# Optimization experiments

Measured on AMD Instinct MI355X. Metric: run time of the kernel, lower is better.

## Reference

```python
import jax, jax.numpy as jnp
import numpy as np

BN_EPS = 1e-5
DIST_EPS = 1e-8


def setup_inputs() -> dict:
    key = jax.random.key(0)
    ks = jax.random.split(key, 8)
    B, N, S = 8, 8192, 2048
    D_unk, D_kn = 128, 256
    inp = {
        "unknown_xyz": jax.random.uniform(ks[0], (B, N, 3), dtype=jnp.float32),
        "known_xyz": jax.random.uniform(ks[1], (B, S, 3), dtype=jnp.float32),
        "unknown_points": jax.random.normal(ks[2], (B, N, D_unk), dtype=jnp.float32),
        "known_points": jax.random.normal(ks[3], (B, S, D_kn), dtype=jnp.float32),
        "W0": jax.random.normal(ks[4], (256, 384), dtype=jnp.float32) * (1.0 / np.sqrt(384)),
        "b0": jnp.zeros((256,), jnp.float32),
        "g0": jnp.ones((256,), jnp.float32),
        "beta0": jnp.zeros((256,), jnp.float32),
        "W1": jax.random.normal(ks[5], (128, 256), dtype=jnp.float32) * (1.0 / np.sqrt(256)),
        "b1": jnp.zeros((128,), jnp.float32),
        "g1": jnp.ones((128,), jnp.float32),
        "beta1": jnp.zeros((128,), jnp.float32),
    }
    return inp


def _three_nn(unknown_xyz, known_xyz):
    # squared pairwise distances [B, N, S]
    d = jnp.sum((unknown_xyz[:, :, None, :] - known_xyz[:, None, :, :]) ** 2, axis=-1)
    neg_top, idx = jax.lax.top_k(-d, 3)  # 3 smallest distances
    return -neg_top, idx  # dists [B,N,3], idx [B,N,3]


def _conv_bn_relu(x, W, b, g, beta):
    # x: [B, N, Cin]; 1x1 Conv1d == per-point linear
    y = jnp.einsum("bnc,oc->bno", x, W) + b
    mean = jnp.mean(y, axis=(0, 1))
    var = jnp.var(y, axis=(0, 1))  # biased, as BatchNorm training forward
    y = g * (y - mean) * jax.lax.rsqrt(var + BN_EPS) + beta
    return jax.nn.relu(y)


def reference(unknown_xyz, known_xyz, unknown_points, known_points,
              W0, b0, g0, beta0, W1, b1, g1, beta1):
    dists, idx = _three_nn(unknown_xyz, known_xyz)
    dist_recip = 1.0 / (dists + DIST_EPS)
    weight = dist_recip / jnp.sum(dist_recip, axis=2, keepdims=True)  # [B,N,3]
    # gather 3 neighbor features: [B,N,3,D_kn]
    gathered = jax.vmap(lambda f, i: f[i])(known_points, idx)
    interpolated = jnp.sum(weight[..., None] * gathered, axis=2)  # [B,N,D_kn]
    x = jnp.concatenate([unknown_points, interpolated], axis=-1)  # [B,N,384]
    x = _conv_bn_relu(x, W0, b0, g0, beta0)
    x = _conv_bn_relu(x, W1, b1, g1, beta1)
    return x  # [B, N, 128]
```

## Files before the change

kernel.cpp:

```cpp
#include <hip/hip_runtime.h>
#include <hip/hip_bf16.h>


typedef __attribute__((ext_vector_type(8))) short short8;
typedef __attribute__((ext_vector_type(4))) float f32x4;

#define BB 8
#define NN 8192
#define SS 2048
#define M_TOT (BB * NN)
#define N1DIM 256
#define K2DIM 256
#define N2DIM 128
#define BK 64

#define GDIM 5
#define NCELL (GDIM * GDIM * GDIM)
#define SLOTS 32
#define CELLW 0.2f

#define KEY_MASK 0xFFFFF800u
#define IDX_MASK 0x7FFu

__device__ __forceinline__ unsigned short f2bf(float f) {
    unsigned int x = __float_as_uint(f);
    unsigned int r = x + 0x7fffu + ((x >> 16) & 1u);
    return (unsigned short)(r >> 16);
}
__device__ __forceinline__ float bf2f(unsigned short u) {
    return __uint_as_float(((unsigned int)u) << 16);
}
__device__ __forceinline__ unsigned int med3_u32(unsigned int a, unsigned int b,
                                                 unsigned int c) {
    unsigned int r;
    asm("v_med3_u32 %0, %1, %2, %3" : "=v"(r) : "v"(a), "v"(b), "v"(c));
    return r;
}

__device__ __forceinline__ void ins5(unsigned int k[5], unsigned int key) {
    unsigned int n1 = med3_u32(k[0], k[1], key);
    unsigned int n2 = med3_u32(k[1], k[2], key);
    unsigned int n3 = med3_u32(k[2], k[3], key);
    unsigned int n4 = med3_u32(k[3], k[4], key);
    k[0] = min(k[0], key);
    k[1] = n1; k[2] = n2; k[3] = n3; k[4] = n4;
}

__device__ __forceinline__ float rescue_write(
    const unsigned int k[5], float qx, float qy, float qz,
    const float4* __restrict__ kpB, uint4* __restrict__ widx, size_t pt)
{
    unsigned long long e[5];
#pragma unroll
    for (int i = 0; i < 5; ++i) {
        if ((k[i] & KEY_MASK) >= 0x7F800000u) {
            e[i] = 0xFFFFFFFFFFFFFFFFull;
        } else {
            unsigned int idx = k[i] & IDX_MASK;
            float4 c = kpB[idx];
            float dx = c.x - qx, dy = c.y - qy, dz = c.z - qz;
            float d = fmaf(dx, dx, fmaf(dy, dy, dz * dz));
            e[i] = ((unsigned long long)__float_as_uint(d) << 32) | idx;
        }
    }
#pragma unroll
    for (int i = 0; i < 3; ++i)
#pragma unroll
        for (int j = i + 1; j < 5; ++j)
            if (e[j] < e[i]) { unsigned long long t = e[i]; e[i] = e[j]; e[j] = t; }

    float d0 = __uint_as_float((unsigned int)(e[0] >> 32));
    float d1 = __uint_as_float((unsigned int)(e[1] >> 32));
    float d2 = __uint_as_float((unsigned int)(e[2] >> 32));
    float r0 = 1.0f / (d0 + 1e-8f);
    float r1 = 1.0f / (d1 + 1e-8f);
    float r2 = 1.0f / (d2 + 1e-8f);
    float rs = 1.0f / (r0 + r1 + r2);
    unsigned int i0 = (unsigned int)(e[0] & IDX_MASK);
    unsigned int i1 = (unsigned int)(e[1] & IDX_MASK);
    unsigned int i2 = (unsigned int)(e[2] & IDX_MASK);
    widx[pt] = make_uint4(__float_as_uint(r0 * rs), __float_as_uint(r1 * rs),
                          i0 | (i1 << 16), i2);
    return d2;
}

__device__ __forceinline__ void gload_lds16(const void* g, void* lds) {
    __builtin_amdgcn_global_load_lds(
        (const __attribute__((address_space(1))) unsigned int*)g,
        (__attribute__((address_space(3))) unsigned int*)lds, 16, 0, 0);
}

__global__ __launch_bounds__(256) void cvt_w_kernel(
    const float* __restrict__ W0, const float* __restrict__ W1,
    const float* __restrict__ kxyz,
    unsigned short* __restrict__ Wa, unsigned short* __restrict__ Wb,
    unsigned short* __restrict__ Wb1, float4* __restrict__ kpack,
    float4* __restrict__ table, int* __restrict__ cnt,
    int* __restrict__ nfail, float* __restrict__ statsF)
{
    int i = blockIdx.x * 256 + threadIdx.x;
    if (blockIdx.x == 0) {
        for (int j = threadIdx.x; j < 768; j += 256) statsF[j] = 0.0f;
        if (threadIdx.x == 0) *nfail = 0;
    }
    if (i < BB * NCELL) cnt[i] = 0;
    if (i < BB * NCELL * SLOTS)
        table[i] = make_float4(1e30f, 1e30f, 1e30f, 0.0f);
    if (i < 256 * 384) {
        int o = i / 384, c = i - o * 384;
        unsigned short v = f2bf(W0[i]);
        if (c < 128) Wa[o * 128 + c] = v;
        else         Wb[o * 256 + (c - 128)] = v;
    }
    if (i < N2DIM * K2DIM) Wb1[i] = f2bf(W1[i]);
    if (i < BB * SS) {
        const float* p = kxyz + (size_t)i * 3;
        float px = p[0], py = p[1], pz = p[2];
        kpack[i] = make_float4(px, py, pz, fmaf(px, px, fmaf(py, py, pz * pz)));
    }
}

__global__ __launch_bounds__(256) void bin_scatter_kernel(
    const float* __restrict__ kxyz, float4* __restrict__ table,
    int* __restrict__ cnt)
{
    int i = blockIdx.x * 256 + threadIdx.x;
    if (i >= BB * SS) return;
    int b = i >> 11, s = i & 2047;
    const float* p = kxyz + (size_t)i * 3;
    float x = p[0], y = p[1], z = p[2];
    int cx = min((int)(x * GDIM), GDIM - 1);
    int cy = min((int)(y * GDIM), GDIM - 1);
    int cz = min((int)(z * GDIM), GDIM - 1);
    int cell = (cz * GDIM + cy) * GDIM + cx;
    int slot = atomicAdd(&cnt[b * NCELL + cell], 1);
    if (slot < SLOTS)
        table[((size_t)(b * NCELL + cell)) * SLOTS + slot] =
            make_float4(x, y, z, __int_as_float(s));
}

__global__ __launch_bounds__(256) void nn_grid_kernel(
    const float* __restrict__ uxyz, const float4* __restrict__ table,
    const int* __restrict__ cnt, const float4* __restrict__ kpack,
    uint4* __restrict__ widx, int* __restrict__ fail_list,
    int* __restrict__ nfail)
{
    const int t  = blockIdx.x * 256 + threadIdx.x;
    const int qd = t & 3;
    const size_t pt = (size_t)(t >> 2);
    const int b = (int)(pt >> 13);

    const float* up = uxyz + pt * 3;
    const float qx = up[0], qy = up[1], qz = up[2];

    const int cx = min((int)(qx * GDIM), GDIM - 1);
    const int cy = min((int)(qy * GDIM), GDIM - 1);
    const int cz = min((int)(qz * GDIM), GDIM - 1);
    const float fx = qx * GDIM - cx, fy = qy * GDIM - cy, fz = qz * GDIM - cz;
    int ox = cx - (fx <= 0.5f ? 1 : 0); ox = max(0, min(ox, GDIM - 2));
    int oy = cy - (fy <= 0.5f ? 1 : 0); oy = max(0, min(oy, GDIM - 2));
    int oz = cz - (fz <= 0.5f ? 1 : 0); oz = max(0, min(oz, GDIM - 2));

    const float4* tb = table + (size_t)b * NCELL * SLOTS;
    const int* cb = cnt + b * NCELL;

    unsigned int k[5] = {0xFFFFFFFFu, 0xFFFFFFFFu, 0xFFFFFFFFu,
                         0xFFFFFFFFu, 0xFFFFFFFFu};
    int ovf = 0;
#pragma unroll
    for (int jj = 0; jj < 2; ++jj) {
        const int j = qd * 2 + jj;
        const int dx = j & 1, dy = (j >> 1) & 1, dz = j >> 2;
        const int cell = ((oz + dz) * GDIM + (oy + dy)) * GDIM + (ox + dx);
        ovf |= (cb[cell] > SLOTS) ? 1 : 0;
        const float4* cp = tb + (size_t)cell * SLOTS;
#pragma unroll 8
        for (int s = 0; s < SLOTS; ++s) {
            float4 c = cp[s];
            float ddx = c.x - qx, ddy = c.y - qy, ddz = c.z - qz;
            float d = fmaf(ddx, ddx, fmaf(ddy, ddy, ddz * ddz));
            unsigned int key = (__float_as_uint(d) & KEY_MASK) |
                               (unsigned int)__float_as_int(c.w);
            ins5(k, key);
        }
    }

#pragma unroll
    for (int m = 1; m <= 2; m <<= 1) {
        unsigned int f0 = (unsigned int)__shfl_xor((int)k[0], m);
        unsigned int f1 = (unsigned int)__shfl_xor((int)k[1], m);
        unsigned int f2 = (unsigned int)__shfl_xor((int)k[2], m);
        unsigned int f3 = (unsigned int)__shfl_xor((int)k[3], m);
        unsigned int f4 = (unsigned int)__shfl_xor((int)k[4], m);
        ovf |= __shfl_xor(ovf, m);
        ins5(k, f0); ins5(k, f1); ins5(k, f2); ins5(k, f3); ins5(k, f4);
    }

    if (qd != 0) return;

    float d3 = rescue_write(k, qx, qy, qz, kpack + (size_t)b * SS, widx, pt);

    float lx = ox * CELLW, rx = (ox + 2) * CELLW;
    float ly = oy * CELLW, ry = (oy + 2) * CELLW;
    float lz = oz * CELLW, rz = (oz + 2) * CELLW;
    float covx = fminf(ox == 0 ? 1e30f : qx - lx, ox == GDIM - 2 ? 1e30f : rx - qx);
    float covy = fminf(oy == 0 ? 1e30f : qy - ly, oy == GDIM - 2 ? 1e30f : ry - qy);
    float covz = fminf(oz == 0 ? 1e30f : qz - lz, oz == GDIM - 2 ? 1e30f : rz - qz);
    float g = fminf(covx, fminf(covy, covz));

    if (ovf || !(d3 <= g * g)) {
        int pos = atomicAdd(nfail, 1);
        fail_list[pos] = (int)pt;
    }
}

__global__ __launch_bounds__(256) void nn_brute_kernel(
    const float* __restrict__ uxyz, const float4* __restrict__ kpack,
    const int* __restrict__ fail_list, const int* __restrict__ nfail,
    uint4* __restrict__ widx)
{
    const int l = threadIdx.x & 63;
    const int wv = (blockIdx.x * 256 + threadIdx.x) >> 6;
    const int nw = (gridDim.x * 256) >> 6;
    const int n = *nfail;

    for (int q = wv; q < n; q += nw) {
        const size_t pt = (size_t)fail_list[q];
        const int b = (int)(pt >> 13);
        const float* up = uxyz + pt * 3;
        const float qx = up[0], qy = up[1], qz = up[2];
        const float4* kp = kpack + (size_t)b * SS;

        unsigned int k[5] = {0xFFFFFFFFu, 0xFFFFFFFFu, 0xFFFFFFFFu,
                             0xFFFFFFFFu, 0xFFFFFFFFu};
#pragma unroll 4
        for (int s = l; s < SS; s += 64) {
            float4 c = kp[s];
            float ddx = c.x - qx, ddy = c.y - qy, ddz = c.z - qz;
            float d = fmaf(ddx, ddx, fmaf(ddy, ddy, ddz * ddz));
            unsigned int key = (__float_as_uint(d) & KEY_MASK) | (unsigned int)s;
            ins5(k, key);
        }
#pragma unroll
        for (int m = 1; m <= 32; m <<= 1) {
            unsigned int f0 = (unsigned int)__shfl_xor((int)k[0], m);
            unsigned int f1 = (unsigned int)__shfl_xor((int)k[1], m);
            unsigned int f2 = (unsigned int)__shfl_xor((int)k[2], m);
            unsigned int f3 = (unsigned int)__shfl_xor((int)k[3], m);
            unsigned int f4 = (unsigned int)__shfl_xor((int)k[4], m);
            ins5(k, f0); ins5(k, f1); ins5(k, f2); ins5(k, f3); ins5(k, f4);
        }
        if (l == 0)
            rescue_write(k, qx, qy, qz, kp, widx, pt);
    }
}

__global__ __launch_bounds__(512, 4) void zgemm_kernel(
    const float* __restrict__ kpts,
    const unsigned short* __restrict__ Wb,
    unsigned short* __restrict__ Z)
{
    __shared__ __align__(128) unsigned char smem[2 * 32768];

    const int tid = threadIdx.x;
    const int l = tid & 63, w = tid >> 6;
    const int wm = w >> 2, wn = w & 3;
    const int mt = blockIdx.x >> 1, nh = blockIdx.x & 1;
    const int row0 = mt * 128;
    const int srow = l >> 3, sbo = (l & 7) * 16;
    const int lr = tid >> 2, lcq = tid & 3;

    f32x4 acc[4][2];
#pragma unroll
    for (int m = 0; m < 4; ++m)
#pragma unroll
        for (int n = 0; n < 2; ++n) {
            f32x4 z = {0.f, 0.f, 0.f, 0.f};
            acc[m][n] = z;
        }

    const unsigned char* Bb = (const unsigned char*)Wb + (size_t)nh * 128 * 512;
    float4 af0, af1, af2, af3;

    auto issueA = [&](int t) {
        const float* src = kpts + (size_t)(row0 + lr) * 256 + t * 64 + lcq * 16;
        af0 = ((const float4*)src)[0];
        af1 = ((const float4*)src)[1];
        af2 = ((const float4*)src)[2];
        af3 = ((const float4*)src)[3];
    };
    auto stageB = [&](int buf, int t) {
        unsigned char* Bl = smem + buf * 32768 + 16384;
#pragma unroll
        for (int i = 0; i < 2; ++i) {
            const int r = w * 16 + i * 8 + srow;
            gload_lds16(Bb + (size_t)r * 512 + t * 128 + (sbo ^ ((r & 7) << 4)),
                        Bl + r * 128 + sbo);
        }
    };
    auto xformA = [&](int buf) {
        unsigned char* Al = smem + buf * 32768;
        short8 o0, o1;
        o0[0] = (short)f2bf(af0.x); o0[1] = (short)f2bf(af0.y);
        o0[2] = (short)f2bf(af0.z); o0[3] = (short)f2bf(af0.w);
        o0[4] = (short)f2bf(af1.x); o0[5] = (short)f2bf(af1.y);
        o0[6] = (short)f2bf(af1.z); o0[7] = (short)f2bf(af1.w);
        o1[0] = (short)f2bf(af2.x); o1[1] = (short)f2bf(af2.y);
        o1[2] = (short)f2bf(af2.z); o1[3] = (short)f2bf(af2.w);
        o1[4] = (short)f2bf(af3.x); o1[5] = (short)f2bf(af3.y);
        o1[6] = (short)f2bf(af3.z); o1[7] = (short)f2bf(af3.w);
        const int bo = lcq * 32;
        *(short8*)(Al + lr * 128 + ((bo) ^ ((lr & 7) << 4))) = o0;
        *(short8*)(Al + lr * 128 + ((bo + 16) ^ ((lr & 7) << 4))) = o1;
    };
    auto compute = [&](int buf) {
        const unsigned char* Al = smem + buf * 32768;
        const unsigned char* Bl = Al + 16384;
#pragma unroll
        for (int ks = 0; ks < 2; ++ks) {
            const int bo = ks * 64 + (l >> 4) * 16;
            short8 a[4], bq[2];
#pragma unroll
            for (int m = 0; m < 4; ++m) {
                const int r = wm * 64 + m * 16 + (l & 15);
                a[m] = *(const short8*)(Al + r * 128 + (bo ^ ((r & 7) << 4)));
            }
#pragma unroll
            for (int n = 0; n < 2; ++n) {
                const int r = wn * 32 + n * 16 + (l & 15);
                bq[n] = *(const short8*)(Bl + r * 128 + (bo ^ ((r & 7) << 4)));
            }
#pragma unroll
            for (int m = 0; m < 4; ++m)
#pragma unroll
                for (int n = 0; n < 2; ++n)
                    acc[m][n] = __builtin_amdgcn_mfma_f32_16x16x32_bf16(
                        a[m], bq[n], acc[m][n], 0, 0, 0);
        }
    };

    issueA(0);
    stageB(0, 0);
    xformA(0);
    __syncthreads();
#pragma unroll
    for (int t = 0; t < 4; ++t) {
        const int cur = t & 1;
        if (t + 1 < 4) { issueA(t + 1); stageB(cur ^ 1, t + 1); }
        compute(cur);
        if (t + 1 < 4) xformA(cur ^ 1);
        __syncthreads();
    }

#pragma unroll
    for (int m = 0; m < 4; ++m) {
        const int row = row0 + wm * 64 + m * 16 + (l >> 4) * 4;
#pragma unroll
        for (int n = 0; n < 2; ++n) {
            const int col = nh * 128 + wn * 32 + n * 16 + (l & 15);
            f32x4 v = acc[m][n];
#pragma unroll
            for (int r = 0; r < 4; ++r)
                Z[(size_t)(row + r) * 256 + col] = f2bf(v[r]);
        }
    }
}

__global__ __launch_bounds__(256) void interp_z_kernel(
    const uint4* __restrict__ widx,
    const unsigned short* __restrict__ Z,
    unsigned short* __restrict__ xz)
{
    __shared__ int   sidx[64][3];
    __shared__ float sw[64][3];

    const int tid = threadIdx.x;
    const int bid = blockIdx.x;
    const int b   = bid & 7;
    const int pn  = (bid >> 3) * 64;

    if (tid < 64) {
        uint4 wv = widx[(size_t)b * NN + pn + tid];
        float w0 = __uint_as_float(wv.x);
        float w1 = __uint_as_float(wv.y);
        sidx[tid][0] = (int)(wv.z & 0xFFFFu);
        sidx[tid][1] = (int)(wv.z >> 16);
        sidx[tid][2] = (int)wv.w;
        sw[tid][0] = w0; sw[tid][1] = w1; sw[tid][2] = 1.0f - w0 - w1;
    }
    __syncthreads();

    const int wvv = tid >> 6, lane = tid & 63;
    const unsigned short* Zb = Z + (size_t)b * SS * 256;
    for (int p = wvv; p < 64; p += 4) {
        const int j0 = sidx[p][0], j1 = sidx[p][1], j2 = sidx[p][2];
        const float w0 = sw[p][0], w1 = sw[p][1], w2 = sw[p][2];

        ushort4 z0 = *(const ushort4*)(Zb + (size_t)j0 * 256 + lane * 4);
        ushort4 z1 = *(const ushort4*)(Zb + (size_t)j1 * 256 + lane * 4);
        ushort4 z2 = *(const ushort4*)(Zb + (size_t)j2 * 256 + lane * 4);
        ushort4 o;
        o.x = f2bf(fmaf(w2, bf2f(z2.x), fmaf(w1, bf2f(z1.x), w0 * bf2f(z0.x))));
        o.y = f2bf(fmaf(w2, bf2f(z2.y), fmaf(w1, bf2f(z1.y), w0 * bf2f(z0.y))));
        o.z = f2bf(fmaf(w2, bf2f(z2.z), fmaf(w1, bf2f(z1.z), w0 * bf2f(z0.z))));
        o.w = f2bf(fmaf(w2, bf2f(z2.w), fmaf(w1, bf2f(z1.w), w0 * bf2f(z0.w))));
        *(ushort4*)(xz + ((size_t)b * NN + pn + p) * 256 + lane * 4) = o;
    }
}

__global__ __launch_bounds__(512, 4) void gemm1z_kernel(
    const float* __restrict__ upts,
    const unsigned short* __restrict__ Wa,
    const unsigned short* __restrict__ xz,
    unsigned short* __restrict__ Y0,
    float* __restrict__ stats)
{
    __shared__ __align__(128) unsigned char smem[65536];

    const int tid = threadIdx.x;
    const int l = tid & 63, w = tid >> 6;
    const int wm = w >> 2, wn = w & 3;
    const int mt = blockIdx.x >> 1, nh = blockIdx.x & 1;
    const int row0 = mt * 128;
    const int srow = l >> 3, sbo = (l & 7) * 16;
    const int lr = tid >> 2, lcq = tid & 3;

    {
        const unsigned char* Bb = (const unsigned char*)Wa + (size_t)nh * 128 * 256;
#pragma unroll
        for (int h = 0; h < 2; ++h)
#pragma unroll
            for (int i = 0; i < 2; ++i) {
                const int r = w * 16 + i * 8 + srow;
                gload_lds16(Bb + (size_t)r * 256 + h * 128 + (sbo ^ ((r & 7) << 4)),
                            smem + 32768 + h * 16384 + r * 128 + sbo);
            }
    }
    {
        const float* src = upts + (size_t)(row0 + lr) * 128 + lcq * 32;
        float4 f[8];
#pragma unroll
        for (int q = 0; q < 8; ++q) f[q] = ((const float4*)src)[q];
        unsigned char* Ah = smem + (lcq >> 1) * 16384;
        const int cb = (lcq & 1) * 64;
#pragma unroll
        for (int q = 0; q < 4; ++q) {
            float4 fa = f[q * 2], fb = f[q * 2 + 1];
            short8 o;
            o[0] = (short)f2bf(fa.x); o[1] = (short)f2bf(fa.y);
            o[2] = (short)f2bf(fa.z); o[3] = (short)f2bf(fa.w);
            o[4] = (short)f2bf(fb.x); o[5] = (short)f2bf(fb.y);
            o[6] = (short)f2bf(fb.z); o[7] = (short)f2bf(fb.w);
            *(short8*)(Ah + lr * 128 + ((cb + q * 16) ^ ((lr & 7) << 4))) = o;
        }
    }
    __syncthreads();

    f32x4 acc[4][2];
#pragma unroll
    for (int m = 0; m < 4; ++m)
#pragma unroll
        for (int n = 0; n < 2; ++n) {
            f32x4 z = {0.f, 0.f, 0.f, 0.f};
            acc[m][n] = z;
        }
#pragma unroll
    for (int ks = 0; ks < 4; ++ks) {
        const unsigned char* Al = smem + (ks >> 1) * 16384;
        const unsigned char* Bl = smem + 32768 + (ks >> 1) * 16384;
        const int bo = (ks & 1) * 64 + (l >> 4) * 16;
        short8 a[4], bq[2];
#pragma unroll
        for (int m = 0; m < 4; ++m) {
            const int r = wm * 64 + m * 16 + (l & 15);
            a[m] = *(const short8*)(Al + r * 128 + (bo ^ ((r & 7) << 4)));
        }
#pragma unroll
        for (int n = 0; n < 2; ++n) {
            const int r = wn * 32 + n * 16 + (l & 15);
            bq[n] = *(const short8*)(Bl + r * 128 + (bo ^ ((r & 7) << 4)));
        }
#pragma unroll
        for (int m = 0; m < 4; ++m)
#pragma unroll
            for (int n = 0; n < 2; ++n)
                acc[m][n] = __builtin_amdgcn_mfma_f32_16x16x32_bf16(
                    a[m], bq[n], acc[m][n], 0, 0, 0);
    }

    float s1[2] = {0.f, 0.f}, s2[2] = {0.f, 0.f};
#pragma unroll
    for (int m = 0; m < 4; ++m) {
#pragma unroll
        for (int r = 0; r < 4; ++r) {
            const int row = row0 + wm * 64 + m * 16 + (l >> 4) * 4 + r;
#pragma unroll
            for (int n = 0; n < 2; ++n) {
                const int col = nh * 128 + wn * 32 + n * 16 + (l & 15);
                float f = acc[m][n][r] + bf2f(xz[(size_t)row * 256 + col]);
                Y0[(size_t)row * 256 + col] = f2bf(f);
                s1[n] += f;
                s2[n] += f * f;
            }
        }
    }
#pragma unroll
    for (int n = 0; n < 2; ++n) {
        s1[n] += __shfl_xor(s1[n], 16, 64);
        s1[n] += __shfl_xor(s1[n], 32, 64);
        s2[n] += __shfl_xor(s2[n], 16, 64);
        s2[n] += __shfl_xor(s2[n], 32, 64);
    }
    if (l < 16) {
#pragma unroll
        for (int n = 0; n < 2; ++n) {
            const int col = nh * 128 + wn * 32 + n * 16 + l;
            atomicAdd(&stats[col], s1[n]);
            atomicAdd(&stats[N1DIM + col], s2[n]);
        }
    }
}

#define G2_NT (K2DIM / BK)
__global__ __launch_bounds__(512, 4) void gemm2_kernel(
    const unsigned short* __restrict__ Y0,
    const unsigned short* __restrict__ Wb,
    const float* __restrict__ stats0,
    const float* __restrict__ g0,
    const float* __restrict__ beta0,
    unsigned short* __restrict__ Y1,
    float* __restrict__ stats)
{
    __shared__ __align__(128) unsigned char smem[2 * 32768];
    __shared__ float sgm[K2DIM], sga[K2DIM];

    const int tid = threadIdx.x;
    const int l = tid & 63, w = tid >> 6;
    const int wm = w >> 2, wn = w & 3;
    const int row0 = blockIdx.x * 128;
    const int srow = l >> 3;
    const int sbo  = (l & 7) * 16;
    const int lr  = tid >> 2;
    const int lcq = tid & 3;

    f32x4 acc[4][2];
#pragma unroll
    for (int m = 0; m < 4; ++m)
#pragma unroll
        for (int n = 0; n < 2; ++n) {
            f32x4 z = {0.f, 0.f, 0.f, 0.f};
            acc[m][n] = z;
        }

    const unsigned char* Bb = (const unsigned char*)Wb;
    short8 areg0, areg1;

    auto issueA = [&](int t) {
        const unsigned short* src = Y0 + (size_t)(row0 + lr) * K2DIM + t * BK + lcq * 16;
        areg0 = *(const short8*)src;
        areg1 = *(const short8*)(src + 8);
    };
    auto stageB = [&](int buf, int t) {
        unsigned char* Bl = smem + buf * 32768 + 16384;
        const int k0b = t * (BK * 2);
#pragma unroll
        for (int i = 0; i < 2; ++i) {
            const int r = w * 16 + i * 8 + srow;
            gload_lds16(Bb + (size_t)r * (K2DIM * 2) + k0b + (sbo ^ ((r & 7) << 4)),
                        Bl + r * 128 + sbo);
        }
    };
    auto xformA = [&](int buf, int t) {
        unsigned char* Al = smem + buf * 32768;
        const int kb = t * BK + lcq * 16;
        short8 o0, o1;
#pragma unroll
        for (int j = 0; j < 8; ++j) {
            float f = bf2f((unsigned short)areg0[j]);
            f = fmaxf(fmaf(f, sgm[kb + j], sga[kb + j]), 0.f);
            o0[j] = (short)f2bf(f);
            float g = bf2f((unsigned short)areg1[j]);
            g = fmaxf(fmaf(g, sgm[kb + 8 + j], sga[kb + 8 + j]), 0.f);
            o1[j] = (short)f2bf(g);
        }
        const int bo = lcq * 32;
        *(short8*)(Al + lr * 128 + ((bo) ^ ((lr & 7) << 4))) = o0;
        *(short8*)(Al + lr * 128 + ((bo + 16) ^ ((lr & 7) << 4))) = o1;
    };
    auto compute = [&](int buf) {
        const unsigned char* Al = smem + buf * 32768;
        const unsigned char* Bl = Al + 16384;
#pragma unroll
        for (int ks = 0; ks < 2; ++ks) {
            const int bo = ks * 64 + (l >> 4) * 16;
            short8 a[4], bq[2];
#pragma unroll
            for (int m = 0; m < 4; ++m) {
                const int r = wm * 64 + m * 16 + (l & 15);
                a[m] = *(const short8*)(Al + r * 128 + (bo ^ ((r & 7) << 4)));
            }
#pragma unroll
            for (int n = 0; n < 2; ++n) {
                const int r = wn * 32 + n * 16 + (l & 15);
                bq[n] = *(const short8*)(Bl + r * 128 + (bo ^ ((r & 7) << 4)));
            }
#pragma unroll
            for (int m = 0; m < 4; ++m)
#pragma unroll
                for (int n = 0; n < 2; ++n)
                    acc[m][n] = __builtin_amdgcn_mfma_f32_16x16x32_bf16(
                        a[m], bq[n], acc[m][n], 0, 0, 0);
        }
    };

    if (tid < K2DIM) {
        const float inv = 1.0f / (float)M_TOT;
        float mean = stats0[tid] * inv;
        float var  = stats0[N1DIM + tid] * inv - mean * mean;
        float m = g0[tid] * rsqrtf(var + 1e-5f);
        sgm[tid] = m;
        sga[tid] = beta0[tid] - mean * m;
    }
    issueA(0);
    stageB(0, 0);
    __syncthreads();
    xformA(0, 0);
    __syncthreads();

#pragma unroll
    for (int t = 0; t < G2_NT; ++t) {
        const int cur = t & 1;
        if (t + 1 < G2_NT) { issueA(t + 1); stageB(cur ^ 1, t + 1); }
        compute(cur);
        if (t + 1 < G2_NT) xformA(cur ^ 1, t + 1);
        __syncthreads();
    }

    float s1[2] = {0.f, 0.f}, s2[2] = {0.f, 0.f};
#pragma unroll
    for (int m = 0; m < 4; ++m) {
        const int row = row0 + wm * 64 + m * 16 + (l >> 4) * 4;
#pragma unroll
        for (int n = 0; n < 2; ++n) {
            const int col = wn * 32 + n * 16 + (l & 15);
            f32x4 v = acc[m][n];
#pragma unroll
            for (int r = 0; r < 4; ++r) {
                float f = v[r];
                Y1[(size_t)(row + r) * N2DIM + col] = f2bf(f);
                s1[n] += f;
                s2[n] += f * f;
            }
        }
    }
#pragma unroll
    for (int n = 0; n < 2; ++n) {
        s1[n] += __shfl_xor(s1[n], 16, 64);
        s1[n] += __shfl_xor(s1[n], 32, 64);
        s2[n] += __shfl_xor(s2[n], 16, 64);
        s2[n] += __shfl_xor(s2[n], 32, 64);
    }
    if (l < 16) {
#pragma unroll
        for (int n = 0; n < 2; ++n) {
            const int col = wn * 32 + n * 16 + l;
            atomicAdd(&stats[col], s1[n]);
            atomicAdd(&stats[N2DIM + col], s2[n]);
        }
    }
}

__global__ __launch_bounds__(256) void bn_out_kernel(
    const unsigned short* __restrict__ Y1, const float* __restrict__ stats1,
    const float* __restrict__ g1, const float* __restrict__ beta1,
    float* __restrict__ out)
{
    __shared__ float sgm[N2DIM], sga[N2DIM];
    const int tid = threadIdx.x;
    if (tid < N2DIM) {
        const float inv = 1.0f / (float)M_TOT;
        float mean = stats1[tid] * inv;
        float var  = stats1[N2DIM + tid] * inv - mean * mean;
        float m = g1[tid] * rsqrtf(var + 1e-5f);
        sgm[tid] = m;
        sga[tid] = beta1[tid] - mean * m;
    }
    __syncthreads();

    const int total = M_TOT * N2DIM / 8;
    for (int i = blockIdx.x * 256 + tid; i < total; i += gridDim.x * 256) {
        short8 v = ((const short8*)Y1)[i];
        const int cg = (i & 15) * 8;
        float4 o1, o2;
        o1.x = fmaxf(fmaf(bf2f((unsigned short)v[0]), sgm[cg + 0], sga[cg + 0]), 0.f);
        o1.y = fmaxf(fmaf(bf2f((unsigned short)v[1]), sgm[cg + 1], sga[cg + 1]), 0.f);
        o1.z = fmaxf(fmaf(bf2f((unsigned short)v[2]), sgm[cg + 2], sga[cg + 2]), 0.f);
        o1.w = fmaxf(fmaf(bf2f((unsigned short)v[3]), sgm[cg + 3], sga[cg + 3]), 0.f);
        o2.x = fmaxf(fmaf(bf2f((unsigned short)v[4]), sgm[cg + 4], sga[cg + 4]), 0.f);
        o2.y = fmaxf(fmaf(bf2f((unsigned short)v[5]), sgm[cg + 5], sga[cg + 5]), 0.f);
        o2.z = fmaxf(fmaf(bf2f((unsigned short)v[6]), sgm[cg + 6], sga[cg + 6]), 0.f);
        o2.w = fmaxf(fmaf(bf2f((unsigned short)v[7]), sgm[cg + 7], sga[cg + 7]), 0.f);
        ((float4*)out)[i * 2]     = o1;
        ((float4*)out)[i * 2 + 1] = o2;
    }
}

extern "C" void kernel_launch(void* const* d_in, const int* in_sizes, int n_in,
                              void* d_out, int out_size, void* d_ws, size_t ws_size,
                              hipStream_t stream)
{
    const float* uxyz  = (const float*)d_in[0];
    const float* kxyz  = (const float*)d_in[1];
    const float* upts  = (const float*)d_in[2];
    const float* kpts  = (const float*)d_in[3];
    const float* W0    = (const float*)d_in[4];
    const float* g0    = (const float*)d_in[6];
    const float* beta0 = (const float*)d_in[7];
    const float* W1    = (const float*)d_in[8];
    const float* g1    = (const float*)d_in[10];
    const float* beta1 = (const float*)d_in[11];
    float* out = (float*)d_out;

    char* ws = (char*)d_ws;
    const size_t off_xz = 0;
    const size_t off_y0 = 33554432;
    const size_t off_z  = 67108864;
    const size_t off_w  = 75497472;

    unsigned short* xz   = (unsigned short*)(ws + off_xz);
    unsigned short* y1   = (unsigned short*)(ws + off_xz);
    unsigned short* y0   = (unsigned short*)(ws + off_y0);
    float4* table    = (float4*)(ws + off_y0);
    int*    cellcnt  = (int*)(ws + off_y0 + 524288);
    int*    nfail    = (int*)(ws + off_y0 + 528384);
    int*    faillist = (int*)(ws + off_y0 + 532480);
    float4* kpack    = (float4*)(ws + off_y0 + 8388608);
    unsigned short* Zb   = (unsigned short*)(ws + off_z);
    unsigned short* wa   = (unsigned short*)(ws + off_w);
    unsigned short* wb   = (unsigned short*)(ws + off_w + 65536);
    unsigned short* wb1  = (unsigned short*)(ws + off_w + 196608);
    float* F = (float*)(ws + off_w + 262144);
    float* stats0 = F;
    float* stats1 = F + 512;
    uint4* widx = (uint4*)(ws + off_w + 270336);

    cvt_w_kernel<<<384, 256, 0, stream>>>(W0, W1, kxyz, wa, wb, wb1, kpack,
                                          table, cellcnt, nfail, F);
    bin_scatter_kernel<<<64, 256, 0, stream>>>(kxyz, table, cellcnt);
    nn_grid_kernel<<<1024, 256, 0, stream>>>(uxyz, table, cellcnt, kpack,
                                             widx, faillist, nfail);
    nn_brute_kernel<<<256, 256, 0, stream>>>(uxyz, kpack, faillist, nfail, widx);
    zgemm_kernel<<<256, 512, 0, stream>>>(kpts, wb, Zb);
    interp_z_kernel<<<1024, 256, 0, stream>>>(widx, Zb, xz);
    gemm1z_kernel<<<1024, 512, 0, stream>>>(upts, wa, xz, y0, stats0);
    gemm2_kernel<<<512, 512, 0, stream>>>(y0, wb1, stats0, g0, beta0, y1, stats1);
    bn_out_kernel<<<2048, 256, 0, stream>>>(y1, stats1, g1, beta1, out);
}
```

Before: 162.8 us.

## Move interpolation add and BN stats into gather kernel after unknown-part GEMM

Reorders the pipeline so the first GEMM computes only the unknown-points contribution and stores it through LDS with coalesced 16-byte writes. A new interpolation kernel gathers the three neighbour Z rows, adds the GEMM result, writes Y0 and accumulates BatchNorm statistics with block-level reduction into per-batch partial sums. This is meant to replace scattered 2-byte epilogue accesses and reduce atomic contention on the stats buffer. It adds an LDS staging pass and a small per-batch reduction in gemm2's prologue.

Measured after the change: 151.5 us. -6.9%, faster.

```diff
diff --git a/kernel.cpp b/kernel.cpp
--- a/kernel.cpp
+++ b/kernel.cpp
@@ -100,7 +100,7 @@
 {
     int i = blockIdx.x * 256 + threadIdx.x;
     if (blockIdx.x == 0) {
-        for (int j = threadIdx.x; j < 768; j += 256) statsF[j] = 0.0f;
+        for (int j = threadIdx.x; j < 4608; j += 256) statsF[j] = 0.0f;
         if (threadIdx.x == 0) *nfail = 0;
     }
     if (i < BB * NCELL) cnt[i] = 0;
@@ -366,54 +366,10 @@
     }
 }
 
-__global__ __launch_bounds__(256) void interp_z_kernel(
-    const uint4* __restrict__ widx,
-    const unsigned short* __restrict__ Z,
-    unsigned short* __restrict__ xz)
-{
-    __shared__ int   sidx[64][3];
-    __shared__ float sw[64][3];
-
-    const int tid = threadIdx.x;
-    const int bid = blockIdx.x;
-    const int b   = bid & 7;
-    const int pn  = (bid >> 3) * 64;
-
-    if (tid < 64) {
-        uint4 wv = widx[(size_t)b * NN + pn + tid];
-        float w0 = __uint_as_float(wv.x);
-        float w1 = __uint_as_float(wv.y);
-        sidx[tid][0] = (int)(wv.z & 0xFFFFu);
-        sidx[tid][1] = (int)(wv.z >> 16);
-        sidx[tid][2] = (int)wv.w;
-        sw[tid][0] = w0; sw[tid][1] = w1; sw[tid][2] = 1.0f - w0 - w1;
-    }
-    __syncthreads();
-
-    const int wvv = tid >> 6, lane = tid & 63;
-    const unsigned short* Zb = Z + (size_t)b * SS * 256;
-    for (int p = wvv; p < 64; p += 4) {
-        const int j0 = sidx[p][0], j1 = sidx[p][1], j2 = sidx[p][2];
-        const float w0 = sw[p][0], w1 = sw[p][1], w2 = sw[p][2];
-
-        ushort4 z0 = *(const ushort4*)(Zb + (size_t)j0 * 256 + lane * 4);
-        ushort4 z1 = *(const ushort4*)(Zb + (size_t)j1 * 256 + lane * 4);
-        ushort4 z2 = *(const ushort4*)(Zb + (size_t)j2 * 256 + lane * 4);
-        ushort4 o;
-        o.x = f2bf(fmaf(w2, bf2f(z2.x), fmaf(w1, bf2f(z1.x), w0 * bf2f(z0.x))));
-        o.y = f2bf(fmaf(w2, bf2f(z2.y), fmaf(w1, bf2f(z1.y), w0 * bf2f(z0.y))));
-        o.z = f2bf(fmaf(w2, bf2f(z2.z), fmaf(w1, bf2f(z1.z), w0 * bf2f(z0.z))));
-        o.w = f2bf(fmaf(w2, bf2f(z2.w), fmaf(w1, bf2f(z1.w), w0 * bf2f(z0.w))));
-        *(ushort4*)(xz + ((size_t)b * NN + pn + p) * 256 + lane * 4) = o;
-    }
-}
-
-__global__ __launch_bounds__(512, 4) void gemm1z_kernel(
+__global__ __launch_bounds__(512, 4) void gemm1u_kernel(
     const float* __restrict__ upts,
     const unsigned short* __restrict__ Wa,
-    const unsigned short* __restrict__ xz,
-    unsigned short* __restrict__ Y0,
-    float* __restrict__ stats)
+    unsigned short* __restrict__ Y0u)
 {
     __shared__ __align__(128) unsigned char smem[65536];
 
@@ -488,36 +444,98 @@
                     a[m], bq[n], acc[m][n], 0, 0, 0);
     }
 
-    float s1[2] = {0.f, 0.f}, s2[2] = {0.f, 0.f};
-#pragma unroll
-    for (int m = 0; m < 4; ++m) {
-#pragma unroll
-        for (int r = 0; r < 4; ++r) {
-            const int row = row0 + wm * 64 + m * 16 + (l >> 4) * 4 + r;
-#pragma unroll
-            for (int n = 0; n < 2; ++n) {
-                const int col = nh * 128 + wn * 32 + n * 16 + (l & 15);
-                float f = acc[m][n][r] + bf2f(xz[(size_t)row * 256 + col]);
-                Y0[(size_t)row * 256 + col] = f2bf(f);
-                s1[n] += f;
-                s2[n] += f * f;
-            }
-        }
-    }
-#pragma unroll
-    for (int n = 0; n < 2; ++n) {
-        s1[n] += __shfl_xor(s1[n], 16, 64);
-        s1[n] += __shfl_xor(s1[n], 32, 64);
-        s2[n] += __shfl_xor(s2[n], 16, 64);
-        s2[n] += __shfl_xor(s2[n], 32, 64);
-    }
-    if (l < 16) {
-#pragma unroll
-        for (int n = 0; n < 2; ++n) {
-            const int col = nh * 128 + wn * 32 + n * 16 + l;
-            atomicAdd(&stats[col], s1[n]);
-            atomicAdd(&stats[N1DIM + col], s2[n]);
-        }
+    __syncthreads();
+    {
+        unsigned short* st = (unsigned short*)smem;
+#pragma unroll
+        for (int m = 0; m < 4; ++m)
+#pragma unroll
+            for (int n = 0; n < 2; ++n)
+#pragma unroll
+                for (int r = 0; r < 4; ++r) {
+                    const int row = wm * 64 + m * 16 + (l >> 4) * 4 + r;
+                    const int col = wn * 32 + n * 16 + (l & 15);
+                    st[row * 136 + col] = f2bf(acc[m][n][r]);
+                }
+    }
+    __syncthreads();
+    {
+        const int row = tid >> 2, cb = (tid & 3) * 32;
+        const unsigned short* st = (const unsigned short*)smem;
+        unsigned short* dst = Y0u + (size_t)(row0 + row) * 256 + nh * 128 + cb;
+#pragma unroll
+        for (int i = 0; i < 4; ++i)
+            *(short8*)(dst + i * 8) = *(const short8*)(st + row * 136 + cb + i * 8);
+    }
+}
+
+__global__ __launch_bounds__(256) void interp_y0_kernel(
+    const uint4* __restrict__ widx,
+    const unsigned short* __restrict__ Z,
+    const unsigned short* __restrict__ Y0u,
+    unsigned short* __restrict__ Y0,
+    float* __restrict__ statsR)
+{
+    __shared__ int   sidx[64][3];
+    __shared__ float sw[64][3];
+    __shared__ float sst[4][512];
+
+    const int tid = threadIdx.x;
+    const int bid = blockIdx.x;
+    const int b   = bid & 7;
+    const int pn  = (bid >> 3) * 64;
+    const int wv = tid >> 6, lane = tid & 63;
+
+    if (tid < 64) {
+        uint4 wq = widx[(size_t)b * NN + pn + tid];
+        float w0 = __uint_as_float(wq.x);
+        float w1 = __uint_as_float(wq.y);
+        sidx[tid][0] = (int)(wq.z & 0xFFFFu);
+        sidx[tid][1] = (int)(wq.z >> 16);
+        sidx[tid][2] = (int)wq.w;
+        sw[tid][0] = w0; sw[tid][1] = w1; sw[tid][2] = 1.0f - w0 - w1;
+    }
+    __syncthreads();
+
+    float s1[4] = {0.f, 0.f, 0.f, 0.f}, s2[4] = {0.f, 0.f, 0.f, 0.f};
+    const unsigned short* Zb = Z + (size_t)b * SS * 256;
+    for (int p = wv; p < 64; p += 4) {
+        const int j0 = sidx[p][0], j1 = sidx[p][1], j2 = sidx[p][2];
+        const float w0 = sw[p][0], w1 = sw[p][1], w2 = sw[p][2];
+        const size_t rb = ((size_t)b * NN + pn + p) * 256 + lane * 4;
+
+        ushort4 z0 = *(const ushort4*)(Zb + (size_t)j0 * 256 + lane * 4);
+        ushort4 z1 = *(const ushort4*)(Zb + (size_t)j1 * 256 + lane * 4);
+        ushort4 z2 = *(const ushort4*)(Zb + (size_t)j2 * 256 + lane * 4);
+        ushort4 u  = *(const ushort4*)(Y0u + rb);
+
+        float f0 = bf2f(u.x) + fmaf(w2, bf2f(z2.x), fmaf(w1, bf2f(z1.x), w0 * bf2f(z0.x)));
+        float f1 = bf2f(u.y) + fmaf(w2, bf2f(z2.y), fmaf(w1, bf2f(z1.y), w0 * bf2f(z0.y)));
+        float f2v = bf2f(u.z) + fmaf(w2, bf2f(z2.z), fmaf(w1, bf2f(z1.z), w0 * bf2f(z0.z)));
+        float f3 = bf2f(u.w) + fmaf(w2, bf2f(z2.w), fmaf(w1, bf2f(z1.w), w0 * bf2f(z0.w)));
+
+        ushort4 o;
+        o.x = f2bf(f0); o.y = f2bf(f1); o.z = f2bf(f2v); o.w = f2bf(f3);
+        *(ushort4*)(Y0 + rb) = o;
+
+        s1[0] += f0;  s2[0] += f0 * f0;
+        s1[1] += f1;  s2[1] += f1 * f1;
+        s1[2] += f2v; s2[2] += f2v * f2v;
+        s1[3] += f3;  s2[3] += f3 * f3;
+    }
+
+#pragma unroll
+    for (int j = 0; j < 4; ++j) {
+        sst[wv][lane * 4 + j] = s1[j];
+        sst[wv][256 + lane * 4 + j] = s2[j];
+    }
+    __syncthreads();
+    {
+        float v = sst[0][tid] + sst[1][tid] + sst[2][tid] + sst[3][tid];
+        float q = sst[0][256 + tid] + sst[1][256 + tid] +
+                  sst[2][256 + tid] + sst[3][256 + tid];
+        atomicAdd(&statsR[b * 512 + tid], v);
+        atomicAdd(&statsR[b * 512 + 256 + tid], q);
     }
 }
 
@@ -525,7 +543,7 @@
 __global__ __launch_bounds__(512, 4) void gemm2_kernel(
     const unsigned short* __restrict__ Y0,
     const unsigned short* __restrict__ Wb,
-    const float* __restrict__ stats0,
+    const float* __restrict__ statsR,
     const float* __restrict__ g0,
     const float* __restrict__ beta0,
     unsigned short* __restrict__ Y1,
@@ -614,9 +632,15 @@
     };
 
     if (tid < K2DIM) {
+        float s = 0.f, q = 0.f;
+#pragma unroll
+        for (int r = 0; r < 8; ++r) {
+            s += statsR[r * 512 + tid];
+            q += statsR[r * 512 + 256 + tid];
+        }
         const float inv = 1.0f / (float)M_TOT;
-        float mean = stats0[tid] * inv;
-        float var  = stats0[N1DIM + tid] * inv - mean * mean;
+        float mean = s * inv;
+        float var  = q * inv - mean * mean;
         float m = g0[tid] * rsqrtf(var + 1e-5f);
         sgm[tid] = m;
         sga[tid] = beta0[tid] - mean * m;
@@ -727,7 +751,7 @@
     const size_t off_z  = 67108864;
     const size_t off_w  = 75497472;
 
-    unsigned short* xz   = (unsigned short*)(ws + off_xz);
+    unsigned short* Y0u  = (unsigned short*)(ws + off_xz);
     unsigned short* y1   = (unsigned short*)(ws + off_xz);
     unsigned short* y0   = (unsigned short*)(ws + off_y0);
     float4* table    = (float4*)(ws + off_y0);
@@ -740,9 +764,9 @@
     unsigned short* wb   = (unsigned short*)(ws + off_w + 65536);
     unsigned short* wb1  = (unsigned short*)(ws + off_w + 196608);
     float* F = (float*)(ws + off_w + 262144);
-    float* stats0 = F;
-    float* stats1 = F + 512;
-    uint4* widx = (uint4*)(ws + off_w + 270336);
+    float* statsR = F;
+    float* stats1 = F + 4096;
+    uint4* widx = (uint4*)(ws + off_w + 262144 + 18432);
 
     cvt_w_kernel<<<384, 256, 0, stream>>>(W0, W1, kxyz, wa, wb, wb1, kpack,
                                           table, cellcnt, nfail, F);
@@ -751,8 +775,8 @@
                                              widx, faillist, nfail);
     nn_brute_kernel<<<256, 256, 0, stream>>>(uxyz, kpack, faillist, nfail, widx);
     zgemm_kernel<<<256, 512, 0, stream>>>(kpts, wb, Zb);
-    interp_z_kernel<<<1024, 256, 0, stream>>>(widx, Zb, xz);
-    gemm1z_kernel<<<1024, 512, 0, stream>>>(upts, wa, xz, y0, stats0);
-    gemm2_kernel<<<512, 512, 0, stream>>>(y0, wb1, stats0, g0, beta0, y1, stats1);
+    gemm1u_kernel<<<1024, 512, 0, stream>>>(upts, wa, Y0u);
+    interp_y0_kernel<<<1024, 256, 0, stream>>>(widx, Zb, Y0u, y0, statsR);
+    gemm2_kernel<<<512, 512, 0, stream>>>(y0, wb1, statsR, g0, beta0, y1, stats1);
     bn_out_kernel<<<2048, 256, 0, stream>>>(y1, stats1, g1, beta1, out);
 }
```
